# Performance work log

Measured on AMD Instinct MI355X. Metric: run time of the kernel, lower is better.

The kernel has to match this reference:

```python
import jax, jax.numpy as jnp
import numpy as np

EPS = 1.0  # global `epsilon` in the original code
B, C, N, T = 4, 32, 256, 288
NUM_PRED, NUM_LOCAL = 12, 12
PERIOD, SHORT, LONG = 24, 12, 48
EMB = 16
RE_K = 5  # ResidualExtrapolate kernel width (num_input)


def const_extrap(x, p):
    # replicate-pad right by p along time
    return jnp.concatenate([x, jnp.repeat(x[..., -1:], p, axis=-1)], axis=-1)


def seasonal_extrap(x, p):
    # circular-pad right by p along time (p <= t)
    return jnp.concatenate([x, x[..., :p]], axis=-1)


def term_norm(x, L):
    # sliding-window mean/var over last axis, window L, replicate-padded left.
    pad1 = [(0, 0)] * 3 + [(1, 0)]
    cs = jnp.pad(jnp.cumsum(x, axis=-1), pad1)
    cs2 = jnp.pad(jnp.cumsum(x * x, axis=-1), pad1)
    mean = (cs[..., L:] - cs[..., :-L]) / L            # (b,c,n,t-L+1)
    var = (cs2[..., L:] - cs2[..., :-L]) / L - mean ** 2 + 1e-5
    padL = [(0, 0)] * 3 + [(L - 1, 0)]
    mean = jnp.pad(mean, padL, mode='edge')
    var = jnp.pad(var, padL, mode='edge')
    out = (x - mean) / jnp.sqrt(var + EPS)
    return out, mean, jnp.sqrt(var)


def seasonal_norm(x, P):
    b, c, n, t = x.shape
    xp = x.reshape(b, c, n, t // P, P)
    mean = xp.mean(3)                                   # (b,c,n,P) per-phase
    var = (xp ** 2).mean(3) - mean ** 2 + 1e-5
    mean = jnp.tile(mean, (1, 1, 1, t // P))
    var = jnp.tile(var, (1, 1, 1, t // P))
    out = (x - mean) / jnp.sqrt(var + EPS)
    return out, mean, jnp.sqrt(var)


def spatial_norm(x, emb):
    n = emb.shape[0]
    adj = emb @ emb.T - 10.0 * jnp.eye(n, dtype=x.dtype)
    adj = jax.nn.softmax(adj, axis=-1)                  # (n,n)
    mean = jnp.einsum('nm,bcmt->bcnt', adj, x)
    var = jnp.einsum('nm,bcmt->bcnt', adj, x * x) - mean ** 2 + 1e-5
    out = (x - mean) / jnp.sqrt(var + EPS)
    return out, mean, jnp.sqrt(var)


def residual_extrap(x, W, bias):
    # Conv2d(c -> c*num_pred, kernel (1, RE_K)) on last RE_K steps, then cat.
    b, c, n, t = x.shape
    y = jnp.einsum('ock,bcnk->bon', W[:, :, 0, :], x[..., -RE_K:]) + bias[None, :, None]
    proj = y.reshape(b, NUM_PRED, c, n).transpose(0, 2, 3, 1)  # (b,c,n,num_pred)
    return jnp.concatenate([x, proj], axis=-1)


def conv_time(x, W, bias):
    y = jax.lax.conv_general_dilated(x, W, (1, 1), 'VALID',
                                     dimension_numbers=('NCHW', 'OIHW', 'NCHW'))
    return y + bias[None, :, None, None]


def conv1x1(x, W, bias):
    return jnp.einsum('oc,bcnt->bont', W[:, :, 0, 0], x) + bias[None, :, None, None]


def setup_inputs() -> dict:
    key = jax.random.key(0)
    ks = jax.random.split(key, 16)
    f32 = jnp.float32

    def w(k, shape, fan_in):
        return jax.random.normal(k, shape, dtype=f32) / np.sqrt(fan_in)

    inp = {
        'x': jax.random.normal(ks[0], (B, C, N, T), dtype=f32),
        'node_embedding': 0.1 * jax.random.normal(ks[1], (N, EMB), dtype=f32),
        'conv1_w': w(ks[6], (C, 13 * C, 1, NUM_LOCAL), 13 * C * NUM_LOCAL),
        'conv1_b': jnp.zeros((C,), f32),
        'conv2_w': w(ks[7], (C, 13 * C, 1, NUM_LOCAL), 13 * C * NUM_LOCAL),
        'conv2_b': jnp.zeros((C,), f32),
        'skip_w': w(ks[8], (C, C, 1, 1), C),
        'skip_b': jnp.zeros((C,), f32),
        'res_w': w(ks[9], (C, C, 1, 1), C),
        'res_b': jnp.zeros((C,), f32),
    }
    for i in range(4):
        inp[f're{i + 1}_w'] = w(ks[2 + i], (C * NUM_PRED, C, 1, RE_K), C * RE_K)
        inp[f're{i + 1}_b'] = jnp.zeros((C * NUM_PRED,), f32)
    return inp


def reference(x, node_embedding, conv1_w, conv1_b, conv2_w, conv2_b,
              skip_w, skip_b, res_w, res_b,
              re1_w, re1_b, re2_w, re2_b, re3_w, re3_b, re4_w, re4_b):
    xs, aux = [], []

    x_proj = const_extrap(x, NUM_PRED)
    zeros = jnp.zeros_like(x_proj)
    xs.append(x_proj); aux.append(zeros)

    x1, lt_mean, lt_std = term_norm(x, LONG)
    xp = residual_extrap(x1, re1_w, re1_b)
    mp, sp = const_extrap(lt_mean, NUM_PRED), const_extrap(lt_std, NUM_PRED)
    xs += [xp, mp, sp]; aux += [zeros, mp, sp]

    x2, se_mean, se_std = seasonal_norm(x1, PERIOD)
    xp = residual_extrap(x2, re2_w, re2_b)
    mp, sp = seasonal_extrap(se_mean, NUM_PRED), seasonal_extrap(se_std, NUM_PRED)
    xs += [xp, mp, sp]; aux += [zeros, mp, sp]

    x3, st_mean, st_std = term_norm(x2, SHORT)
    xp = residual_extrap(x3, re3_w, re3_b)
    mp, sp = const_extrap(st_mean, NUM_PRED), const_extrap(st_std, NUM_PRED)
    xs += [xp, mp, sp]; aux += [zeros, mp, sp]

    x4, sn_mean, sn_std = spatial_norm(x3, node_embedding)
    xp = residual_extrap(x4, re4_w, re4_b)
    mp, sp = const_extrap(sn_mean, NUM_PRED), const_extrap(sn_std, NUM_PRED)
    xs += [xp, mp, sp]; aux += [zeros, mp, sp]

    pad1 = [(0, 0)] * 3 + [(1, 0)]
    x_cat = jnp.pad(jnp.concatenate(xs, axis=1), pad1)      # (b,13c,n,T+P+1)
    a_cat = jnp.pad(jnp.concatenate(aux, axis=1), pad1)

    g1 = conv_time(x_cat, conv1_w, conv1_b)
    g2 = conv_time(x_cat, conv2_w, conv2_b)
    a1 = conv_time(a_cat, conv1_w, conv1_b)
    a2 = conv_time(a_cat, conv2_w, conv2_b)

    prod = g1 * g2
    x_z = conv1x1(prod[..., :-NUM_PRED], res_w, res_b)
    s = conv1x1(prod[..., -NUM_PRED:], skip_w, skip_b)
    s_aux = conv1x1((a1 * a2)[..., -NUM_PRED:], skip_w, skip_b)
    return (x_z, s_aux, s)
```

## Files before the change

kernel.cpp:

```cpp
#include <hip/hip_runtime.h>

typedef unsigned short u16;
typedef __attribute__((ext_vector_type(8))) short short8v;
typedef __attribute__((ext_vector_type(4))) float f32x4;

#define PSTR 304L
#define OFF_SAUX 9109504L
#define OFF_S    9502720L
#define CHSTR (32L*256L*PSTR)

static __device__ __forceinline__ float bf2f(u16 u) {
  return __uint_as_float(((unsigned int)u) << 16);
}
static __device__ __forceinline__ u16 f2bf(float f) {
  unsigned int i = __float_as_uint(f);
  i += 0x7FFFu + ((i >> 16) & 1u);
  return (u16)(i >> 16);
}

static __device__ __forceinline__ void gload16(const void* g, void* l) {
  __builtin_amdgcn_global_load_lds(
      (const __attribute__((address_space(1))) unsigned int*)g,
      (__attribute__((address_space(3))) unsigned int*)l, 16, 0, 0);
}

__global__ __launch_bounds__(256) void k_adj(const float* __restrict__ emb,
                                             u16* __restrict__ adjb) {
  const int row = blockIdx.x;
  const int m = threadIdx.x;
  __shared__ float sred[8];
  float er[16];
#pragma unroll
  for (int e = 0; e < 16; ++e) er[e] = emb[row * 16 + e];
  float d = 0.f;
#pragma unroll
  for (int e = 0; e < 16; ++e) d += er[e] * emb[m * 16 + e];
  if (m == row) d -= 10.f;
  float v = d;
#pragma unroll
  for (int off = 32; off; off >>= 1) v = fmaxf(v, __shfl_xor(v, off, 64));
  const int wid = m >> 6, lane = m & 63;
  if (lane == 0) sred[wid] = v;
  __syncthreads();
  const float mx = fmaxf(fmaxf(sred[0], sred[1]), fmaxf(sred[2], sred[3]));
  const float p = expf(d - mx);
  v = p;
#pragma unroll
  for (int off = 32; off; off >>= 1) v += __shfl_xor(v, off, 64);
  if (lane == 0) sred[4 + wid] = v;
  __syncthreads();
  const float sum = sred[4] + sred[5] + sred[6] + sred[7];
  adjb[row * 256 + m] = f2bf(p / sum);
}

__global__ __launch_bounds__(256) void k_prepw(const float* __restrict__ c1w,
                                               const float* __restrict__ c2w,
                                               u16* __restrict__ wB) {
  const int idx = blockIdx.x * 256 + threadIdx.x;
  if (idx >= 156 * 2048) return;
  const int kk = idx >> 11;
  const int rem = idx & 2047;
  const int j = rem >> 5, chp = rem & 31;
  const int pslot = chp >> 3, chlo = chp & 7;
  const int sl = pslot ^ ((j >> 1) & 3);
  const int ch = sl * 8 + chlo;
  const int g = kk / 12, k = kk - g * 12;
  const int cin = g * 32 + ch;
  const float* src = (j < 32) ? c1w : c2w;
  const int jj = j & 31;
  wB[idx] = f2bf(src[(jj * 416 + cin) * 12 + k]);
}

static __device__ __forceinline__ void wscan2(float& s1, float& s2, int lane) {
#pragma unroll
  for (int off = 1; off < 64; off <<= 1) {
    float a = __shfl_up(s1, off, 64);
    float b = __shfl_up(s2, off, 64);
    if (lane >= off) { s1 += a; s2 += b; }
  }
}

__global__ __launch_bounds__(256) void k_norm(const float* __restrict__ x,
                                              u16* __restrict__ xcat) {
  const int wid = threadIdx.x >> 6, lane = threadIdx.x & 63;
  const long row = (long)blockIdx.x * 4 + wid;
  const int b = (int)(row >> 13);
  const int c = (int)((row >> 8) & 31);
  const int n = (int)(row & 255);
  const float* xr = x + row * 288;
  __shared__ float bufA[4][304], bufB[4][304], cs1[4][312], cs2[4][312], sst[4][80];
  float* bA = bufA[wid];
  float* bB = bufB[wid];
  float* p1 = cs1[wid];
  float* p2 = cs2[wid];
  float* psm = sst[wid];
  float* psi = sst[wid] + 24;
  float* psd = sst[wid] + 48;
  const long chb = (long)b * 416 * 256 + n;

  for (int j = 0; j < 5; ++j) { int t = j * 64 + lane; if (t < 288) bA[t] = xr[t]; }

  auto scanbuf = [&](float* src) {
    float ca = 0.f, cb = 0.f;
    if (lane == 0) { p1[0] = 0.f; p2[0] = 0.f; }
    for (int j = 0; j < 5; ++j) {
      int t = j * 64 + lane;
      float v = (t < 288) ? src[t] : 0.f;
      float s1 = v, s2 = v * v;
      wscan2(s1, s2, lane);
      if (t < 288) { p1[t + 1] = ca + s1; p2[t + 1] = cb + s2; }
      ca += __shfl(s1, 63, 64);
      cb += __shfl(s2, 63, 64);
    }
  };

  scanbuf(bA);
  for (int j = 0; j < 5; ++j) {
    int t = j * 64 + lane; if (t >= 288) continue;
    float S, Q;
    if (t >= 47) { S = p1[t + 1] - p1[t - 47]; Q = p2[t + 1] - p2[t - 47]; }
    else         { S = p1[48];                 Q = p2[48]; }
    float m = S * (1.f / 48.f);
    float var = Q * (1.f / 48.f) - m * m + 1e-5f;
    float sd = sqrtf(var);
    float iv = rsqrtf(var + 1.f);
    float xv = bA[t];
    float x1 = (xv - m) * iv;
    bB[t] = x1;
    xcat[(chb + (long)(c)      * 256) * PSTR + 1 + t] = f2bf(xv);
    xcat[(chb + (long)(32 + c) * 256) * PSTR + 1 + t] = f2bf(x1);
    xcat[(chb + (long)(64 + c) * 256) * PSTR + 1 + t] = f2bf(m);
    xcat[(chb + (long)(96 + c) * 256) * PSTR + 1 + t] = f2bf(sd);
  }
  {
    float S = p1[288] - p1[240], Q = p2[288] - p2[240];
    float m = S * (1.f / 48.f);
    float var = Q * (1.f / 48.f) - m * m + 1e-5f;
    float sd = sqrtf(var);
    if (lane < 12) {
      xcat[(chb + (long)(c)      * 256) * PSTR + 289 + lane] = f2bf(bA[287]);
      xcat[(chb + (long)(64 + c) * 256) * PSTR + 289 + lane] = f2bf(m);
      xcat[(chb + (long)(96 + c) * 256) * PSTR + 289 + lane] = f2bf(sd);
    }
    if (lane == 0) {
      xcat[(chb + (long)(c)      * 256) * PSTR] = 0;
      xcat[(chb + (long)(32 + c) * 256) * PSTR] = 0;
      xcat[(chb + (long)(64 + c) * 256) * PSTR] = 0;
      xcat[(chb + (long)(96 + c) * 256) * PSTR] = 0;
    }
  }
  if (lane < 24) {
    float S = 0.f, Q = 0.f;
#pragma unroll
    for (int i2 = 0; i2 < 12; ++i2) { float v = bB[lane + 24 * i2]; S += v; Q += v * v; }
    float m = S * (1.f / 12.f);
    float var = Q * (1.f / 12.f) - m * m + 1e-5f;
    psm[lane] = m; psi[lane] = rsqrtf(var + 1.f); psd[lane] = sqrtf(var);
  }
  for (int j = 0; j < 5; ++j) {
    int t = j * 64 + lane; if (t >= 288) continue;
    int ph = t % 24;
    float m = psm[ph];
    float x2v = (bB[t] - m) * psi[ph];
    bA[t] = x2v;
    xcat[(chb + (long)(128 + c) * 256) * PSTR + 1 + t] = f2bf(x2v);
    xcat[(chb + (long)(160 + c) * 256) * PSTR + 1 + t] = f2bf(m);
    xcat[(chb + (long)(192 + c) * 256) * PSTR + 1 + t] = f2bf(psd[ph]);
  }
  if (lane < 12) {
    xcat[(chb + (long)(160 + c) * 256) * PSTR + 289 + lane] = f2bf(psm[lane]);
    xcat[(chb + (long)(192 + c) * 256) * PSTR + 289 + lane] = f2bf(psd[lane]);
  }
  if (lane == 0) {
    xcat[(chb + (long)(128 + c) * 256) * PSTR] = 0;
    xcat[(chb + (long)(160 + c) * 256) * PSTR] = 0;
    xcat[(chb + (long)(192 + c) * 256) * PSTR] = 0;
  }
  scanbuf(bA);
  for (int j = 0; j < 5; ++j) {
    int t = j * 64 + lane; if (t >= 288) continue;
    float S, Q;
    if (t >= 11) { S = p1[t + 1] - p1[t - 11]; Q = p2[t + 1] - p2[t - 11]; }
    else         { S = p1[12];                 Q = p2[12]; }
    float m = S * (1.f / 12.f);
    float var = Q * (1.f / 12.f) - m * m + 1e-5f;
    float sd = sqrtf(var);
    float iv = rsqrtf(var + 1.f);
    float x3v = (bA[t] - m) * iv;
    xcat[(chb + (long)(224 + c) * 256) * PSTR + 1 + t] = f2bf(x3v);
    xcat[(chb + (long)(256 + c) * 256) * PSTR + 1 + t] = f2bf(m);
    xcat[(chb + (long)(288 + c) * 256) * PSTR + 1 + t] = f2bf(sd);
  }
  {
    float S = p1[288] - p1[276], Q = p2[288] - p2[276];
    float m = S * (1.f / 12.f);
    float var = Q * (1.f / 12.f) - m * m + 1e-5f;
    float sd = sqrtf(var);
    if (lane < 12) {
      xcat[(chb + (long)(256 + c) * 256) * PSTR + 289 + lane] = f2bf(m);
      xcat[(chb + (long)(288 + c) * 256) * PSTR + 289 + lane] = f2bf(sd);
    }
    if (lane == 0) {
      xcat[(chb + (long)(224 + c) * 256) * PSTR] = 0;
      xcat[(chb + (long)(256 + c) * 256) * PSTR] = 0;
      xcat[(chb + (long)(288 + c) * 256) * PSTR] = 0;
    }
  }
}

__global__ __launch_bounds__(256) void k_re(u16* __restrict__ xcat,
                                            const float* __restrict__ W,
                                            const float* __restrict__ bias,
                                            int srcch) {
  const long gid = (long)blockIdx.x * 256 + threadIdx.x;
  const int o = (int)(gid % 384);
  const long bn = gid / 384;
  const int n = (int)(bn & 255);
  const int b = (int)(bn >> 8);
  const float* wr = W + o * 160;
  float acc = bias[o];
  for (int c = 0; c < 32; ++c) {
    const long rb = ((long)(b * 416 + srcch + c) * 256 + n) * PSTR + 284;
#pragma unroll
    for (int k = 0; k < 5; ++k) acc += wr[c * 5 + k] * bf2f(xcat[rb + k]);
  }
  const int cd = o & 31, p = o >> 5;
  xcat[((long)(b * 416 + srcch + cd) * 256 + n) * PSTR + 289 + p] = f2bf(acc);
}

__global__ __launch_bounds__(256) void k_spatial(u16* __restrict__ xcat,
                                                 const u16* __restrict__ adjb) {
  const int gx = blockIdx.x;
  const int tcn = gx >> 2, ncb = gx & 3;
  const int slice = blockIdx.y;
  const int b = slice >> 5, c = slice & 31;
  const int t0 = tcn * 64, n0 = ncb * 64;
  const int tid = threadIdx.x;
  const int wid = tid >> 6, lane = tid & 63;
  const int wm = wid >> 1, wn = wid & 1;
  const int l15 = lane & 15, lq = lane >> 4;
  __shared__ __align__(16) u16 BT[2][64 * 40];
  __shared__ __align__(16) u16 BT2[2][64 * 40];
  const f32x4 vz = {0.f, 0.f, 0.f, 0.f};
  f32x4 aM[2][2], aV[2][2];
#pragma unroll
  for (int i = 0; i < 2; ++i)
#pragma unroll
    for (int j = 0; j < 2; ++j) { aM[i][j] = vz; aV[i][j] = vz; }
  const long base7 = (long)(b * 416 + 224 + c) * 256;
  u16 rv[8];
#pragma unroll
  for (int r = 0; r < 8; ++r) {
    int idx = tid + r * 256; int ml = idx >> 6, s = idx & 63;
    rv[r] = xcat[(base7 + ml) * PSTR + 1 + t0 + s];
  }
#pragma unroll
  for (int r = 0; r < 8; ++r) {
    int idx = tid + r * 256; int ml = idx >> 6, s = idx & 63;
    float v = bf2f(rv[r]);
    BT[0][s * 40 + ml] = rv[r];
    BT2[0][s * 40 + ml] = f2bf(v * v);
  }
  __syncthreads();
  int cur = 0;
  for (int kk = 0; kk < 8; ++kk) {
    u16 rn[8];
    if (kk < 7) {
#pragma unroll
      for (int r = 0; r < 8; ++r) {
        int idx = tid + r * 256; int ml = idx >> 6, s = idx & 63;
        rn[r] = xcat[(base7 + (long)((kk + 1) * 32 + ml)) * PSTR + 1 + t0 + s];
      }
    }
    const short8v a0 = *(const short8v*)(adjb + (long)(n0 + wm * 32 + l15) * 256 + kk * 32 + lq * 8);
    const short8v a1 = *(const short8v*)(adjb + (long)(n0 + wm * 32 + 16 + l15) * 256 + kk * 32 + lq * 8);
    const u16* bt = BT[cur];
    const u16* bq = BT2[cur];
    const short8v b0 = *(const short8v*)(bt + (wn * 32 + l15) * 40 + lq * 8);
    const short8v b1 = *(const short8v*)(bt + (wn * 32 + 16 + l15) * 40 + lq * 8);
    const short8v q0 = *(const short8v*)(bq + (wn * 32 + l15) * 40 + lq * 8);
    const short8v q1 = *(const short8v*)(bq + (wn * 32 + 16 + l15) * 40 + lq * 8);
    aM[0][0] = __builtin_amdgcn_mfma_f32_16x16x32_bf16(a0, b0, aM[0][0], 0, 0, 0);
    aM[0][1] = __builtin_amdgcn_mfma_f32_16x16x32_bf16(a0, b1, aM[0][1], 0, 0, 0);
    aM[1][0] = __builtin_amdgcn_mfma_f32_16x16x32_bf16(a1, b0, aM[1][0], 0, 0, 0);
    aM[1][1] = __builtin_amdgcn_mfma_f32_16x16x32_bf16(a1, b1, aM[1][1], 0, 0, 0);
    aV[0][0] = __builtin_amdgcn_mfma_f32_16x16x32_bf16(a0, q0, aV[0][0], 0, 0, 0);
    aV[0][1] = __builtin_amdgcn_mfma_f32_16x16x32_bf16(a0, q1, aV[0][1], 0, 0, 0);
    aV[1][0] = __builtin_amdgcn_mfma_f32_16x16x32_bf16(a1, q0, aV[1][0], 0, 0, 0);
    aV[1][1] = __builtin_amdgcn_mfma_f32_16x16x32_bf16(a1, q1, aV[1][1], 0, 0, 0);
    __syncthreads();
    if (kk < 7) {
#pragma unroll
      for (int r = 0; r < 8; ++r) {
        int idx = tid + r * 256; int ml = idx >> 6, s = idx & 63;
        float v = bf2f(rn[r]);
        BT[cur ^ 1][s * 40 + ml] = rn[r];
        BT2[cur ^ 1][s * 40 + ml] = f2bf(v * v);
      }
    }
    __syncthreads();
    cur ^= 1;
  }
#pragma unroll
  for (int mf = 0; mf < 2; ++mf)
#pragma unroll
    for (int nf = 0; nf < 2; ++nf)
#pragma unroll
      for (int e = 0; e < 4; ++e) {
        const int i = wm * 32 + mf * 16 + lq * 4 + e;
        const int j = wn * 32 + nf * 16 + l15;
        const int nn = n0 + i, tt2 = t0 + j;
        if (tt2 < 288) {
          const float mean = aM[mf][nf][e], ex2 = aV[mf][nf][e];
          const float var = ex2 - mean * mean + 1e-5f;
          const float sd = sqrtf(var);
          const float iv = rsqrtf(var + 1.f);
          const float x3c = bf2f(xcat[(base7 + nn) * PSTR + 1 + tt2]);
          const float x4 = (x3c - mean) * iv;
          const long r10 = ((long)(b * 416 + 320 + c) * 256 + nn) * PSTR;
          const long r11 = ((long)(b * 416 + 352 + c) * 256 + nn) * PSTR;
          const long r12 = ((long)(b * 416 + 384 + c) * 256 + nn) * PSTR;
          xcat[r10 + 1 + tt2] = f2bf(x4);
          xcat[r11 + 1 + tt2] = f2bf(mean);
          xcat[r12 + 1 + tt2] = f2bf(sd);
          if (tt2 == 287) {
            for (int p = 0; p < 12; ++p) {
              xcat[r11 + 289 + p] = f2bf(mean);
              xcat[r12 + 289 + p] = f2bf(sd);
            }
          }
          if (tt2 == 0) { xcat[r10] = 0; xcat[r11] = 0; xcat[r12] = 0; }
        }
      }
}

__global__ __launch_bounds__(256, 3) void k_convG(
    const u16* __restrict__ xcat, const u16* __restrict__ wB,
    const float* __restrict__ c1b, const float* __restrict__ c2b,
    const float* __restrict__ rsw, const float* __restrict__ rsb,
    const float* __restrict__ skw, const float* __restrict__ skb,
    float* __restrict__ out) {
  const int tc = blockIdx.x;
  const int by = blockIdx.y;
  const int b = by >> 6;
  const int tid = threadIdx.x;
  const int wid = tid >> 6, lane = tid & 63;
  const int n_abs = (by & 63) * 4 + wid;
  const int t0 = tc * 64;
  const int l15 = lane & 15, lq = lane >> 4;

  __shared__ __align__(16) unsigned char smem[41984];
  u16* Asm = (u16*)smem;
  u16* Bsm = (u16*)(smem + 25600);

  int sch[5], stk[5];
  const u16* baseR[5];
#pragma unroll
  for (int r = 0; r < 5; ++r) {
    int cc = r * 64 + lane;
    int s = cc / 10;
    int tk = cc - s * 10;
    sch[r] = s; stk[r] = tk;
    baseR[r] = xcat + ((long)(b * 416 + s) * 256 + n_abs) * PSTR + t0 + tk * 8;
  }
  u16* aw = Asm + wid * 3200;

  uint4 aR[5];
#pragma unroll
  for (int r = 0; r < 5; ++r) aR[r] = *(const uint4*)baseR[r];
#pragma unroll
  for (int r = 0; r < 5; ++r) {
    u16 pc[8]; *(uint4*)pc = aR[r];
#pragma unroll
    for (int e = 0; e < 8; ++e) aw[(stk[r] * 8 + e) * 40 + sch[r]] = pc[e];
  }
#pragma unroll
  for (int r = 0; r < 5; ++r) aR[r] = *(const uint4*)(baseR[r] + CHSTR);
  gload16(wB + 0 * 2048 + wid * 512 + lane * 8, Bsm + 0 + wid * 512);
  gload16(wB + 1 * 2048 + wid * 512 + lane * 8, Bsm + 2048 + wid * 512);
  __syncthreads();

  const f32x4 vz = {0.f, 0.f, 0.f, 0.f};
  f32x4 acc[4][4];
#pragma unroll
  for (int i = 0; i < 4; ++i)
#pragma unroll
    for (int j = 0; j < 4; ++j) acc[i][j] = vz;

  const u16* awl = aw + l15 * 40;
  const u16* bwl = Bsm + l15 * 32 + ((lq ^ ((l15 >> 1) & 3)) << 3);

  int p = 0;
  for (int g = 0; g < 13; ++g) {
    for (int kp = 0; kp < 6; ++kp) {
      if (p < 77) {
        const long kkn = (long)(p + 1) * 2;
        const int bufn = ((p + 1) & 1) * 4096;
        gload16(wB + kkn * 2048 + wid * 512 + lane * 8, Bsm + bufn + wid * 512);
        gload16(wB + (kkn + 1) * 2048 + wid * 512 + lane * 8, Bsm + bufn + 2048 + wid * 512);
      }
      const int bufc = (p & 1) * 4096;
#pragma unroll
      for (int kh = 0; kh < 2; ++kh) {
        const int K = kp * 2 + kh;
        short8v af[4], bf[4];
#pragma unroll
        for (int f = 0; f < 4; ++f)
          af[f] = *(const short8v*)(awl + (K + f * 16) * 40 + lq * 8);
#pragma unroll
        for (int f = 0; f < 4; ++f)
          bf[f] = *(const short8v*)(bwl + bufc + kh * 2048 + f * 512);
#pragma unroll
        for (int i = 0; i < 4; ++i)
#pragma unroll
          for (int j = 0; j < 4; ++j)
            acc[i][j] = __builtin_amdgcn_mfma_f32_16x16x32_bf16(af[i], bf[j], acc[i][j], 0, 0, 0);
      }
      __syncthreads();
      ++p;
    }
    if (g < 12) {
#pragma unroll
      for (int r = 0; r < 5; ++r) {
        u16 pc[8]; *(uint4*)pc = aR[r];
#pragma unroll
        for (int e = 0; e < 8; ++e) aw[(stk[r] * 8 + e) * 40 + sch[r]] = pc[e];
      }
      if (g < 11) {
#pragma unroll
        for (int r = 0; r < 5; ++r) aR[r] = *(const uint4*)(baseR[r] + (long)(g + 2) * CHSTR);
      }
    }
  }

  float* pw = (float*)smem + wid * 2112;
#pragma unroll
  for (int fi = 0; fi < 4; ++fi)
#pragma unroll
    for (int nf = 0; nf < 2; ++nf)
#pragma unroll
      for (int e = 0; e < 4; ++e) {
        const int trow = fi * 16 + lq * 4 + e;
        const int cch = nf * 16 + l15;
        const float g1 = acc[fi][nf][e] + c1b[cch];
        const float g2 = acc[fi][nf + 2][e] + c2b[cch];
        pw[trow * 33 + cch] = g1 * g2;
      }
  float pv[32];
  {
    const float* prow = pw + lane * 33;
#pragma unroll
    for (int c = 0; c < 32; ++c) pv[c] = prow[c];
  }
  const int t = t0 + lane;
  if (t0 + 63 < 278) {
    for (int o = 0; o < 32; ++o) {
      float s = rsb[o];
      const float* wr = rsw + o * 32;
#pragma unroll
      for (int c = 0; c < 32; ++c) s += wr[c] * pv[c];
      out[((long)(b * 32 + o) * 256 + n_abs) * 278 + t] = s;
    }
  } else {
    const bool isres = t < 278;
    const bool isskip = (t >= 278) && (t < 290);
    for (int o = 0; o < 32; ++o) {
      const float* wr = (isres ? rsw : skw) + o * 32;
      float s = (isres ? rsb : skb)[o];
#pragma unroll
      for (int c = 0; c < 32; ++c) s += wr[c] * pv[c];
      if (isres)       out[((long)(b * 32 + o) * 256 + n_abs) * 278 + t] = s;
      else if (isskip) out[OFF_S + ((long)(b * 32 + o) * 256 + n_abs) * 12 + (t - 278)] = s;
    }
  }
}

__global__ __launch_bounds__(256) void k_convA(const u16* __restrict__ xcat,
    const u16* __restrict__ wB, const float* __restrict__ c1b,
    const float* __restrict__ c2b, const float* __restrict__ skw,
    const float* __restrict__ skb, float* __restrict__ out) {
  const int tid = threadIdx.x;
  const int wid = tid >> 6, lane = tid & 63;
  const int row = blockIdx.x * 4 + wid;
  const int b = row >> 8, n = row & 255;
  const int l15 = lane & 15, lq = lane >> 4;
  __shared__ __align__(16) u16 ATa[4][32 * 40];
  __shared__ float apL[4][16 * 65];
  u16* at = ATa[wid];
  float* ap = apL[wid];
  const f32x4 vz = {0.f, 0.f, 0.f, 0.f};
  f32x4 acc[4] = {vz, vz, vz, vz};
  const long bnbase = (long)b * 416 * 256 + n;
  const int bsw = (lq ^ ((l15 >> 1) & 3)) << 3;
  for (int gi = 0; gi < 8; ++gi) {
    const int g = 2 + 3 * (gi >> 1) + (gi & 1);
#pragma unroll
    for (int r = 0; r < 14; ++r) {
      int idx = lane + r * 64;
      int ci = idx / 28, s = idx - ci * 28;
      at[s * 40 + ci] = xcat[(bnbase + (long)(g * 32 + ci) * 256) * PSTR + 278 + s];
    }
    for (int k = 0; k < 12; ++k) {
      const short8v af = *(const short8v*)(at + (l15 + k) * 40 + lq * 8);
#pragma unroll
      for (int nf = 0; nf < 4; ++nf) {
        const short8v bf = *(const short8v*)(wB + (long)(g * 12 + k) * 2048 + (nf * 16 + l15) * 32 + bsw);
        acc[nf] = __builtin_amdgcn_mfma_f32_16x16x32_bf16(af, bf, acc[nf], 0, 0, 0);
      }
    }
  }
#pragma unroll
  for (int nf = 0; nf < 4; ++nf)
#pragma unroll
    for (int e = 0; e < 4; ++e)
      ap[(lq * 4 + e) * 65 + nf * 16 + l15] = acc[nf][e];
  for (int r = 0; r < 6; ++r) {
    const int task = lane + r * 64;
    const int o = task & 31, tt = task >> 5;
    float s = skb[o];
#pragma unroll
    for (int c2 = 0; c2 < 32; ++c2)
      s += skw[o * 32 + c2] * (ap[tt * 65 + c2] + c1b[c2]) * (ap[tt * 65 + 32 + c2] + c2b[c2]);
    out[OFF_SAUX + ((long)(b * 32 + o) * 256 + n) * 12 + tt] = s;
  }
}

extern "C" void kernel_launch(void* const* d_in, const int* in_sizes, int n_in,
                              void* d_out, int out_size, void* d_ws, size_t ws_size,
                              hipStream_t stream) {
  const float* x   = (const float*)d_in[0];
  const float* emb = (const float*)d_in[1];
  const float* c1w = (const float*)d_in[2];
  const float* c1b = (const float*)d_in[3];
  const float* c2w = (const float*)d_in[4];
  const float* c2b = (const float*)d_in[5];
  const float* skw = (const float*)d_in[6];
  const float* skb = (const float*)d_in[7];
  const float* rsw = (const float*)d_in[8];
  const float* rsb = (const float*)d_in[9];
  float* out = (float*)d_out;

  u16* xcat = (u16*)d_ws;
  u16* wB   = xcat + (4L * 416 * 256 * 304 + 2048);
  u16* adjb = wB + 156L * 2048;

  k_adj<<<dim3(256), dim3(256), 0, stream>>>(emb, adjb);
  k_prepw<<<dim3(1248), dim3(256), 0, stream>>>(c1w, c2w, wB);
  k_norm<<<dim3(8192), dim3(256), 0, stream>>>(x, xcat);
  k_re<<<dim3(1536), dim3(256), 0, stream>>>(xcat, (const float*)d_in[10], (const float*)d_in[11], 32);
  k_re<<<dim3(1536), dim3(256), 0, stream>>>(xcat, (const float*)d_in[12], (const float*)d_in[13], 128);
  k_re<<<dim3(1536), dim3(256), 0, stream>>>(xcat, (const float*)d_in[14], (const float*)d_in[15], 224);
  k_spatial<<<dim3(20, 128), dim3(256), 0, stream>>>(xcat, adjb);
  k_re<<<dim3(1536), dim3(256), 0, stream>>>(xcat, (const float*)d_in[16], (const float*)d_in[17], 320);
  k_convG<<<dim3(5, 256), dim3(256), 0, stream>>>(xcat, wB, c1b, c2b, rsw, rsb, skw, skb, out);
  k_convA<<<dim3(256), dim3(256), 0, stream>>>(xcat, wB, c1b, c2b, skw, skb, out);
}
```

Before: 699.6 us.

## Merge independent launches into fused multi-role kernels and swizzle conv A tile

Collapses ten kernel launches into four by dispatching on block index: norm, adj and weight prep share one front kernel. Spatial norm runs alongside the first three residual-extrapolation jobs, and the gated conv and aux conv share one grid. The conv A-tile LDS writes and reads now use an XOR swizzle on the column to cut bank conflicts, and a barrier is added before the epilogue reuses shared memory. This removes launch gaps and tail idle time, at the cost of shared register/LDS limits across roles; convA now runs under the convG occupancy bound.

```diff
diff --git a/kernel.cpp b/kernel.cpp
--- a/kernel.cpp
+++ b/kernel.cpp
@@ -24,9 +24,8 @@
       (__attribute__((address_space(3))) unsigned int*)l, 16, 0, 0);
 }
 
-__global__ __launch_bounds__(256) void k_adj(const float* __restrict__ emb,
-                                             u16* __restrict__ adjb) {
-  const int row = blockIdx.x;
+static __device__ void adj_body(int row, const float* __restrict__ emb,
+                                u16* __restrict__ adjb) {
   const int m = threadIdx.x;
   __shared__ float sred[8];
   float er[16];
@@ -53,11 +52,10 @@
   adjb[row * 256 + m] = f2bf(p / sum);
 }
 
-__global__ __launch_bounds__(256) void k_prepw(const float* __restrict__ c1w,
-                                               const float* __restrict__ c2w,
-                                               u16* __restrict__ wB) {
-  const int idx = blockIdx.x * 256 + threadIdx.x;
-  if (idx >= 156 * 2048) return;
+static __device__ void prepw_body(int bid, const float* __restrict__ c1w,
+                                  const float* __restrict__ c2w,
+                                  u16* __restrict__ wB) {
+  const int idx = bid * 256 + threadIdx.x;
   const int kk = idx >> 11;
   const int rem = idx & 2047;
   const int j = rem >> 5, chp = rem & 31;
@@ -80,10 +78,10 @@
   }
 }
 
-__global__ __launch_bounds__(256) void k_norm(const float* __restrict__ x,
-                                              u16* __restrict__ xcat) {
+static __device__ void norm_body(int bid, const float* __restrict__ x,
+                                 u16* __restrict__ xcat) {
   const int wid = threadIdx.x >> 6, lane = threadIdx.x & 63;
-  const long row = (long)blockIdx.x * 4 + wid;
+  const long row = (long)bid * 4 + wid;
   const int b = (int)(row >> 13);
   const int c = (int)((row >> 8) & 31);
   const int n = (int)(row & 255);
@@ -208,11 +206,19 @@
   }
 }
 
-__global__ __launch_bounds__(256) void k_re(u16* __restrict__ xcat,
-                                            const float* __restrict__ W,
-                                            const float* __restrict__ bias,
-                                            int srcch) {
-  const long gid = (long)blockIdx.x * 256 + threadIdx.x;
+__global__ __launch_bounds__(256) void k_front(const float* __restrict__ x,
+    const float* __restrict__ emb, const float* __restrict__ c1w,
+    const float* __restrict__ c2w, u16* __restrict__ xcat,
+    u16* __restrict__ adjb, u16* __restrict__ wB) {
+  const int bid = blockIdx.x;
+  if (bid < 8192)       norm_body(bid, x, xcat);
+  else if (bid < 8448)  adj_body(bid - 8192, emb, adjb);
+  else                  prepw_body(bid - 8448, c1w, c2w, wB);
+}
+
+static __device__ void re_body(long gid, u16* __restrict__ xcat,
+                               const float* __restrict__ W,
+                               const float* __restrict__ bias, int srcch) {
   const int o = (int)(gid % 384);
   const long bn = gid / 384;
   const int n = (int)(bn & 255);
@@ -228,11 +234,17 @@
   xcat[((long)(b * 416 + srcch + cd) * 256 + n) * PSTR + 289 + p] = f2bf(acc);
 }
 
-__global__ __launch_bounds__(256) void k_spatial(u16* __restrict__ xcat,
-                                                 const u16* __restrict__ adjb) {
-  const int gx = blockIdx.x;
+__global__ __launch_bounds__(256) void k_re4(u16* __restrict__ xcat,
+                                             const float* __restrict__ W,
+                                             const float* __restrict__ bias) {
+  re_body((long)blockIdx.x * 256 + threadIdx.x, xcat, W, bias, 320);
+}
+
+static __device__ void spatial_body(int sid, u16* __restrict__ xcat,
+                                    const u16* __restrict__ adjb) {
+  const int gx = sid % 20;
+  const int slice = sid / 20;
   const int tcn = gx >> 2, ncb = gx & 3;
-  const int slice = blockIdx.y;
   const int b = slice >> 5, c = slice & 31;
   const int t0 = tcn * 64, n0 = ncb * 64;
   const int tid = threadIdx.x;
@@ -334,14 +346,27 @@
       }
 }
 
-__global__ __launch_bounds__(256, 3) void k_convG(
+__global__ __launch_bounds__(256) void k_mid(u16* __restrict__ xcat,
+    const u16* __restrict__ adjb,
+    const float* __restrict__ w1, const float* __restrict__ b1,
+    const float* __restrict__ w2, const float* __restrict__ b2,
+    const float* __restrict__ w3, const float* __restrict__ b3) {
+  const int bid = blockIdx.x;
+  if (bid < 2560) { spatial_body(bid, xcat, adjb); return; }
+  const int sub = bid - 2560;
+  const int which = sub / 1536;
+  const long gid = (long)(sub - which * 1536) * 256 + threadIdx.x;
+  if (which == 0)      re_body(gid, xcat, w1, b1, 32);
+  else if (which == 1) re_body(gid, xcat, w2, b2, 128);
+  else                 re_body(gid, xcat, w3, b3, 224);
+}
+
+static __device__ void convG_body(int tc, int by,
     const u16* __restrict__ xcat, const u16* __restrict__ wB,
     const float* __restrict__ c1b, const float* __restrict__ c2b,
     const float* __restrict__ rsw, const float* __restrict__ rsb,
     const float* __restrict__ skw, const float* __restrict__ skb,
-    float* __restrict__ out) {
-  const int tc = blockIdx.x;
-  const int by = blockIdx.y;
+    float* __restrict__ out, unsigned char* smem) {
   const int b = by >> 6;
   const int tid = threadIdx.x;
   const int wid = tid >> 6, lane = tid & 63;
@@ -349,7 +374,6 @@
   const int t0 = tc * 64;
   const int l15 = lane & 15, lq = lane >> 4;
 
-  __shared__ __align__(16) unsigned char smem[41984];
   u16* Asm = (u16*)smem;
   u16* Bsm = (u16*)(smem + 25600);
 
@@ -365,15 +389,19 @@
   }
   u16* aw = Asm + wid * 3200;
 
+#define AWRITE() { \
+    _Pragma("unroll") \
+    for (int r = 0; r < 5; ++r) { \
+      u16 pc[8]; *(uint4*)pc = aR[r]; \
+      const int pcol = ((((sch[r] >> 3) ^ stk[r]) & 3) << 3) + (sch[r] & 7); \
+      _Pragma("unroll") \
+      for (int e = 0; e < 8; ++e) aw[(stk[r] * 8 + e) * 40 + pcol] = pc[e]; \
+    } }
+
   uint4 aR[5];
 #pragma unroll
   for (int r = 0; r < 5; ++r) aR[r] = *(const uint4*)baseR[r];
-#pragma unroll
-  for (int r = 0; r < 5; ++r) {
-    u16 pc[8]; *(uint4*)pc = aR[r];
-#pragma unroll
-    for (int e = 0; e < 8; ++e) aw[(stk[r] * 8 + e) * 40 + sch[r]] = pc[e];
-  }
+  AWRITE();
 #pragma unroll
   for (int r = 0; r < 5; ++r) aR[r] = *(const uint4*)(baseR[r] + CHSTR);
   gload16(wB + 0 * 2048 + wid * 512 + lane * 8, Bsm + 0 + wid * 512);
@@ -387,7 +415,6 @@
 #pragma unroll
     for (int j = 0; j < 4; ++j) acc[i][j] = vz;
 
-  const u16* awl = aw + l15 * 40;
   const u16* bwl = Bsm + l15 * 32 + ((lq ^ ((l15 >> 1) & 3)) << 3);
 
   int p = 0;
@@ -405,8 +432,10 @@
         const int K = kp * 2 + kh;
         short8v af[4], bf[4];
 #pragma unroll
-        for (int f = 0; f < 4; ++f)
-          af[f] = *(const short8v*)(awl + (K + f * 16) * 40 + lq * 8);
+        for (int f = 0; f < 4; ++f) {
+          const int tt = K + f * 16 + l15;
+          af[f] = *(const short8v*)(aw + tt * 40 + (((lq ^ (tt >> 3)) & 3) << 3));
+        }
 #pragma unroll
         for (int f = 0; f < 4; ++f)
           bf[f] = *(const short8v*)(bwl + bufc + kh * 2048 + f * 512);
@@ -420,18 +449,15 @@
       ++p;
     }
     if (g < 12) {
-#pragma unroll
-      for (int r = 0; r < 5; ++r) {
-        u16 pc[8]; *(uint4*)pc = aR[r];
-#pragma unroll
-        for (int e = 0; e < 8; ++e) aw[(stk[r] * 8 + e) * 40 + sch[r]] = pc[e];
-      }
+      AWRITE();
       if (g < 11) {
 #pragma unroll
         for (int r = 0; r < 5; ++r) aR[r] = *(const uint4*)(baseR[r] + (long)(g + 2) * CHSTR);
       }
     }
   }
+#undef AWRITE
+  __syncthreads();
 
   float* pw = (float*)smem + wid * 2112;
 #pragma unroll
@@ -475,19 +501,18 @@
   }
 }
 
-__global__ __launch_bounds__(256) void k_convA(const u16* __restrict__ xcat,
+static __device__ void convA_body(int blk, const u16* __restrict__ xcat,
     const u16* __restrict__ wB, const float* __restrict__ c1b,
     const float* __restrict__ c2b, const float* __restrict__ skw,
-    const float* __restrict__ skb, float* __restrict__ out) {
+    const float* __restrict__ skb, float* __restrict__ out,
+    unsigned char* smem) {
   const int tid = threadIdx.x;
   const int wid = tid >> 6, lane = tid & 63;
-  const int row = blockIdx.x * 4 + wid;
+  const int row = blk * 4 + wid;
   const int b = row >> 8, n = row & 255;
   const int l15 = lane & 15, lq = lane >> 4;
-  __shared__ __align__(16) u16 ATa[4][32 * 40];
-  __shared__ float apL[4][16 * 65];
-  u16* at = ATa[wid];
-  float* ap = apL[wid];
+  u16* at = (u16*)smem + wid * 1280;
+  float* ap = (float*)(smem + 10240) + wid * 1040;
   const f32x4 vz = {0.f, 0.f, 0.f, 0.f};
   f32x4 acc[4] = {vz, vz, vz, vz};
   const long bnbase = (long)b * 416 * 256 + n;
@@ -523,6 +548,19 @@
       s += skw[o * 32 + c2] * (ap[tt * 65 + c2] + c1b[c2]) * (ap[tt * 65 + 32 + c2] + c2b[c2]);
     out[OFF_SAUX + ((long)(b * 32 + o) * 256 + n) * 12 + tt] = s;
   }
+}
+
+__global__ __launch_bounds__(256, 3) void k_convGA(
+    const u16* __restrict__ xcat, const u16* __restrict__ wB,
+    const float* __restrict__ c1b, const float* __restrict__ c2b,
+    const float* __restrict__ rsw, const float* __restrict__ rsb,
+    const float* __restrict__ skw, const float* __restrict__ skb,
+    float* __restrict__ out) {
+  __shared__ __align__(16) unsigned char smem[41984];
+  if (blockIdx.x < 5)
+    convG_body(blockIdx.x, blockIdx.y, xcat, wB, c1b, c2b, rsw, rsb, skw, skb, out, smem);
+  else
+    convA_body(blockIdx.y, xcat, wB, c1b, c2b, skw, skb, out, smem);
 }
 
 extern "C" void kernel_launch(void* const* d_in, const int* in_sizes, int n_in,
@@ -544,14 +582,11 @@
   u16* wB   = xcat + (4L * 416 * 256 * 304 + 2048);
   u16* adjb = wB + 156L * 2048;
 
-  k_adj<<<dim3(256), dim3(256), 0, stream>>>(emb, adjb);
-  k_prepw<<<dim3(1248), dim3(256), 0, stream>>>(c1w, c2w, wB);
-  k_norm<<<dim3(8192), dim3(256), 0, stream>>>(x, xcat);
-  k_re<<<dim3(1536), dim3(256), 0, stream>>>(xcat, (const float*)d_in[10], (const float*)d_in[11], 32);
-  k_re<<<dim3(1536), dim3(256), 0, stream>>>(xcat, (const float*)d_in[12], (const float*)d_in[13], 128);
-  k_re<<<dim3(1536), dim3(256), 0, stream>>>(xcat, (const float*)d_in[14], (const float*)d_in[15], 224);
-  k_spatial<<<dim3(20, 128), dim3(256), 0, stream>>>(xcat, adjb);
-  k_re<<<dim3(1536), dim3(256), 0, stream>>>(xcat, (const float*)d_in[16], (const float*)d_in[17], 320);
-  k_convG<<<dim3(5, 256), dim3(256), 0, stream>>>(xcat, wB, c1b, c2b, rsw, rsb, skw, skb, out);
-  k_convA<<<dim3(256), dim3(256), 0, stream>>>(xcat, wB, c1b, c2b, skw, skb, out);
-}
+  k_front<<<dim3(9696), dim3(256), 0, stream>>>(x, emb, c1w, c2w, xcat, adjb, wB);
+  k_mid<<<dim3(7168), dim3(256), 0, stream>>>(xcat, adjb,
+      (const float*)d_in[10], (const float*)d_in[11],
+      (const float*)d_in[12], (const float*)d_in[13],
+      (const float*)d_in[14], (const float*)d_in[15]);
+  k_re4<<<dim3(1536), dim3(256), 0, stream>>>(xcat, (const float*)d_in[16], (const float*)d_in[17]);
+  k_convGA<<<dim3(6, 256), dim3(256), 0, stream>>>(xcat, wB, c1b, c2b, rsw, rsb, skw, skb, out);
+}
```

Measured after the change: 665.0 us. -4.9%, faster.
